# Kernel tuning notes

Measured on AMD Instinct MI355X. Metric: run time of the kernel, lower is better.

Reference implementation:

```python
import jax, jax.numpy as jnp
import numpy as np

N_NODES = 50000
N_EDGES = 600000
D_IN = 128
D_HID = 128
N_IDX = 4096


def gcn_conv(x, W, b, edge_index, num_nodes):
    """PyG GCNConv: add self loops, symmetric deg normalization, scatter-add, bias."""
    h = x @ W  # [N, D_out]
    loop = jnp.arange(num_nodes, dtype=edge_index.dtype)
    src = jnp.concatenate([edge_index[0], loop])
    dst = jnp.concatenate([edge_index[1], loop])
    deg = jax.ops.segment_sum(jnp.ones_like(dst, dtype=h.dtype), dst, num_segments=num_nodes)
    dinv = jnp.where(deg > 0, jax.lax.rsqrt(jnp.maximum(deg, 1.0)), 0.0)
    norm = dinv[src] * dinv[dst]  # [E+N]
    msgs = h[src] * norm[:, None]
    out = jax.ops.segment_sum(msgs, dst, num_segments=num_nodes)
    return out + b


def setup_inputs() -> dict:
    key = jax.random.key(0)
    ks = jax.random.split(key, 18)
    d = {
        "x": jax.random.normal(ks[0], (N_NODES, D_IN), dtype=jnp.float32),
        "syntactic_edge_index": jax.random.randint(ks[1], (2, N_EDGES), 0, N_NODES, dtype=jnp.int32),
        "sequential_edge_index": jax.random.randint(ks[2], (2, N_EDGES), 0, N_NODES, dtype=jnp.int32),
        "semantic_edge_index": jax.random.randint(ks[3], (2, N_EDGES), 0, N_NODES, dtype=jnp.int32),
        "index": jax.random.randint(ks[4], (N_IDX,), 0, N_NODES, dtype=jnp.int32),
    }
    s = 1.0 / np.sqrt(D_IN)
    names = ["syn", "seq", "sem"]
    for i, n in enumerate(names):
        d[f"w1_{n}"] = jax.random.uniform(ks[5 + i], (D_IN, D_HID), jnp.float32, -s, s)
        d[f"b1_{n}"] = jnp.zeros((D_HID,), jnp.float32)
        d[f"w2_{n}"] = jax.random.uniform(ks[8 + i], (D_HID, D_HID), jnp.float32, -s, s)
        d[f"b2_{n}"] = jnp.zeros((D_HID,), jnp.float32)
    return d


def reference(x, syntactic_edge_index, sequential_edge_index, semantic_edge_index, index,
              w1_syn, b1_syn, w1_seq, b1_seq, w1_sem, b1_sem,
              w2_syn, b2_syn, w2_seq, b2_seq, w2_sem, b2_sem):
    n = x.shape[0]
    # layer 1: three parallel GCN branches + ReLU (dropout is identity in eval mode)
    a = jax.nn.relu(gcn_conv(x, w1_syn, b1_syn, syntactic_edge_index, n))
    b = jax.nn.relu(gcn_conv(x, w1_seq, b1_seq, sequential_edge_index, n))
    c = jax.nn.relu(gcn_conv(x, w1_sem, b1_sem, semantic_edge_index, n))
    h = jnp.maximum(jnp.maximum(a, b), c)
    # layer 2
    a2 = jax.nn.relu(gcn_conv(h, w2_syn, b2_syn, syntactic_edge_index, n))
    b2 = jax.nn.relu(gcn_conv(h, w2_seq, b2_seq, sequential_edge_index, n))
    c2 = jax.nn.relu(gcn_conv(h, w2_sem, b2_sem, semantic_edge_index, n))
    out = jnp.maximum(jnp.maximum(a2, b2), c2)
    return out[index]
```

## Files before the change

kernel.cpp:

```cpp
#include <hip/hip_runtime.h>
#include <hip/hip_fp16.h>

#define NN 50000
#define NE 600000
#define NG 3
#define D  128
#define NI 4096
#define BW 1024
#define NBUCK 49
#define EPT_BIN 16
#define EPB_BIN (256 * EPT_BIN)
#define NBLK_BIN ((NE + EPB_BIN - 1) / EPB_BIN)
#define XCVT_BLKS 3125
#define WCVT_BLKS 48
#define CNT_BLKS (NBLK_BIN * NG)

typedef _Float16 half8 __attribute__((ext_vector_type(8)));
typedef _Float16 half4v __attribute__((ext_vector_type(4)));
typedef float floatx4 __attribute__((ext_vector_type(4)));

static __device__ __forceinline__ float wextract(unsigned int v) {
  unsigned short u = (unsigned short)(v >> 16);
  _Float16 h;
  __builtin_memcpy(&h, &u, 2);
  return (float)h;
}

static __device__ __forceinline__ unsigned int packsw(int s, float w) {
  _Float16 h = (_Float16)w;
  unsigned short u;
  __builtin_memcpy(&u, &h, 2);
  return (unsigned int)s | ((unsigned int)u << 16);
}


__global__ __launch_bounds__(256) void prep_kernel(
    const float* __restrict__ x, __half* __restrict__ xh,
    const float* __restrict__ W0, const float* __restrict__ W1, const float* __restrict__ W2,
    const float* __restrict__ W3, const float* __restrict__ W4, const float* __restrict__ W5,
    __half* __restrict__ Wf,
    const int* __restrict__ e0, const int* __restrict__ e1, const int* __restrict__ e2,
    int* __restrict__ bucketCnt) {
  __shared__ int cnt[NBUCK];
  int blk = blockIdx.x;
  int tid = threadIdx.x;
  if (blk < XCVT_BLKS) {
    int i = blk * 256 + tid;
    size_t base = (size_t)i * 8;
    float4 v0 = *(const float4*)&x[base];
    float4 v1 = *(const float4*)&x[base + 4];
    half8 h;
    h[0] = (_Float16)v0.x; h[1] = (_Float16)v0.y; h[2] = (_Float16)v0.z; h[3] = (_Float16)v0.w;
    h[4] = (_Float16)v1.x; h[5] = (_Float16)v1.y; h[6] = (_Float16)v1.z; h[7] = (_Float16)v1.w;
    *(half8*)&xh[base] = h;
  } else if (blk < XCVT_BLKS + WCVT_BLKS) {
    const float* Wm[6] = {W0, W1, W2, W3, W4, W5};
    int t = (blk - XCVT_BLKS) * 256 + tid;
    int mat = t >> 11;
    int fr = (t >> 6) & 31;
    int lane = t & 63;
    int tt = fr >> 2, ks = fr & 3;
    int n = tt * 16 + (lane & 15);
    int kb = ks * 32 + (lane >> 4) * 8;
    const float* W = Wm[mat];
#pragma unroll
    for (int j = 0; j < 8; j++)
      Wf[(size_t)t * 8 + j] = __float2half(W[(kb + j) * 128 + n]);
  } else {
    int cb = blk - XCVT_BLKS - WCVT_BLKS;
    int g = cb / NBLK_BIN, eb = cb % NBLK_BIN;
    const int* ei = (g == 0) ? e0 : ((g == 1) ? e1 : e2);
    if (tid < NBUCK) cnt[tid] = 0;
    __syncthreads();
    int base = eb * EPB_BIN;
#pragma unroll
    for (int i = 0; i < EPT_BIN; i++) {
      int e = base + tid + i * 256;
      if (e < NE) atomicAdd(&cnt[ei[NE + e] >> 10], 1);
    }
    __syncthreads();
    if (tid < NBUCK) atomicAdd(&bucketCnt[g * NBUCK + tid], cnt[tid]);
  }
}

__global__ void bscan_kernel(const int* __restrict__ bucketCnt, int* __restrict__ bucketBase,
                             int* __restrict__ cursor, int* __restrict__ rp) {
  int g = threadIdx.x >> 6;
  int lane = threadIdx.x & 63;
  if (g >= NG) return;
  int v = (lane < NBUCK) ? bucketCnt[g * NBUCK + lane] : 0;
  int incl = v;
#pragma unroll
  for (int off = 1; off < 64; off <<= 1) {
    int t = __shfl_up(incl, off, 64);
    if (lane >= off) incl += t;
  }
  int ex = incl - v;
  if (lane < NBUCK) {
    bucketBase[g * NBUCK + lane] = ex;
    cursor[g * NBUCK + lane] = ex;
  }
  if (lane == 0) rp[g * (NN + 1) + NN] = NE;
}

__global__ __launch_bounds__(256) void bin_kernel(const int* __restrict__ e0,
    const int* __restrict__ e1, const int* __restrict__ e2,
    int* __restrict__ cursor, unsigned int* __restrict__ binned) {
  __shared__ int cnt[4][NBUCK];
  __shared__ int base[NBUCK];
  __shared__ int woff[4][NBUCK];
  int g = blockIdx.y;
  const int* ei = (g == 0) ? e0 : ((g == 1) ? e1 : e2);
  int tid = threadIdx.x;
  int wave = tid >> 6;
  if (tid < NBUCK) { cnt[0][tid] = 0; cnt[1][tid] = 0; cnt[2][tid] = 0; cnt[3][tid] = 0; }
  __syncthreads();
  int estart = blockIdx.x * EPB_BIN;
  int src[EPT_BIN], dst[EPT_BIN], rk[EPT_BIN];
#pragma unroll
  for (int i = 0; i < EPT_BIN; i++) {
    int e = estart + tid + i * 256;
    if (e < NE) {
      src[i] = ei[e];
      dst[i] = ei[NE + e];
      rk[i] = atomicAdd(&cnt[wave][dst[i] >> 10], 1);
    } else {
      rk[i] = -1;
    }
  }
  __syncthreads();
  if (tid < NBUCK) {
    int c0 = cnt[0][tid], c1 = cnt[1][tid], c2 = cnt[2][tid], c3 = cnt[3][tid];
    int total = c0 + c1 + c2 + c3;
    base[tid] = (total > 0) ? atomicAdd(&cursor[g * NBUCK + tid], total) : 0;
    woff[0][tid] = 0; woff[1][tid] = c0; woff[2][tid] = c0 + c1; woff[3][tid] = c0 + c1 + c2;
  }
  __syncthreads();
#pragma unroll
  for (int i = 0; i < EPT_BIN; i++) {
    if (rk[i] >= 0) {
      int b = dst[i] >> 10;
      binned[(size_t)g * NE + base[b] + woff[wave][b] + rk[i]] =
          (unsigned int)src[i] | ((unsigned int)dst[i] << 16);
    }
  }
}

__global__ __launch_bounds__(256) void csr_kernel(const unsigned int* __restrict__ binned,
    const int* __restrict__ bucketBase, const int* __restrict__ bucketCnt,
    int* __restrict__ rp, float* __restrict__ dinv) {
  __shared__ int deg[BW];
  __shared__ int wsum[4];
  int g = blockIdx.y, b = blockIdx.x;
  int tid = threadIdx.x;
  int node0 = b * BW;
  int bb = bucketBase[g * NBUCK + b];
  int total = bucketCnt[g * NBUCK + b];
  const unsigned int* bp = binned + (size_t)g * NE + bb;
  for (int i = tid; i < BW; i += 256) deg[i] = 0;
  __syncthreads();
  for (int e = tid; e < total; e += 256) {
    unsigned int p = bp[e];
    atomicAdd(&deg[(int)(p >> 16) - node0], 1);
  }
  __syncthreads();
  int d0 = deg[tid * 4], d1 = deg[tid * 4 + 1], d2 = deg[tid * 4 + 2], d3 = deg[tid * 4 + 3];
  int s = d0 + d1 + d2 + d3;
  int lane = tid & 63;
  int incl = s;
#pragma unroll
  for (int off = 1; off < 64; off <<= 1) {
    int n = __shfl_up(incl, off, 64);
    if (lane >= off) incl += n;
  }
  if (lane == 63) wsum[tid >> 6] = incl;
  __syncthreads();
  int wbase = 0;
#pragma unroll
  for (int w = 0; w < 4; w++)
    if (w < (tid >> 6)) wbase += wsum[w];
  int ex = wbase + incl - s;
  int exs[4] = {ex, ex + d0, ex + d0 + d1, ex + d0 + d1 + d2};
  int ds[4] = {d0, d1, d2, d3};
#pragma unroll
  for (int k = 0; k < 4; k++) {
    int node = node0 + tid * 4 + k;
    if (node < NN) {
      rp[g * (NN + 1) + node] = bb + exs[k];
      dinv[g * NN + node] = rsqrtf((float)ds[k] + 1.0f);
    }
  }
}

__global__ __launch_bounds__(256) void fillp_kernel(const unsigned int* __restrict__ binned,
    const int* __restrict__ bucketBase, const int* __restrict__ bucketCnt,
    const int* __restrict__ rp, const float* __restrict__ dinv,
    unsigned int* __restrict__ colp) {
  __shared__ int cur[BW];
  int g = blockIdx.y, b = blockIdx.x;
  int tid = threadIdx.x;
  int node0 = b * BW;
  int bb = bucketBase[g * NBUCK + b];
  int total = bucketCnt[g * NBUCK + b];
  const unsigned int* bp = binned + (size_t)g * NE + bb;
  for (int i = tid; i < BW; i += 256) {
    int node = node0 + i;
    cur[i] = (node < NN) ? rp[g * (NN + 1) + node] : 0;
  }
  __syncthreads();
  for (int e = tid; e < total; e += 256) {
    unsigned int p = bp[e];
    int srcid = (int)(p & 0xffffu);
    int r = atomicAdd(&cur[(int)(p >> 16) - node0], 1);
    colp[(size_t)g * NE + r] = packsw(srcid, dinv[g * NN + srcid]);
  }
}


__global__ __launch_bounds__(256) void aggb_kernel(
    const __half* __restrict__ srch, const int* __restrict__ rp,
    const unsigned int* __restrict__ colp, const float* __restrict__ dinv,
    const int* __restrict__ index, __half* __restrict__ tout, int nrows) {
  int b = blockIdx.y;
  int lane = threadIdx.x & 63;
  int grp = lane >> 4;
  int l16 = lane & 15;
  int gb = grp << 4;
  int wv = (blockIdx.x * 256 + threadIdx.x) >> 6;
  int w = wv * 4 + grp;
  int valid = (w < nrows);
  int wc = valid ? w : 0;
  int node = index ? index[wc] : wc;
  const _Float16* srcv = (const _Float16*)srch;
  const int* rpb = rp + b * (NN + 1);
  int s = rpb[node];
  int e = rpb[node + 1];
  int n = valid ? (e - s) : 0;
  float di = dinv[b * NN + node];
  half8 selfh = *(const half8*)&srcv[(size_t)node * D + l16 * 8];
  float a[8];
#pragma unroll
  for (int k = 0; k < 8; k++) a[k] = di * (float)selfh[k];
  int nmax = n;
  nmax = max(nmax, __shfl_xor(nmax, 16, 64));
  nmax = max(nmax, __shfl_xor(nmax, 32, 64));
  const unsigned int* cp = colp + (size_t)b * NE;
  for (int j0 = 0; j0 < nmax; j0 += 16) {
    unsigned int c = (j0 + l16 < n) ? cp[s + j0 + l16] : 0u;
    int rem = nmax - j0;
    rem = (rem > 16) ? 16 : rem;
    for (int jj = 0; jj < rem; jj += 4) {
      unsigned int v0 = (unsigned int)__shfl((int)c, gb + jj + 0, 64);
      unsigned int v1 = (unsigned int)__shfl((int)c, gb + jj + 1, 64);
      unsigned int v2 = (unsigned int)__shfl((int)c, gb + jj + 2, 64);
      unsigned int v3 = (unsigned int)__shfl((int)c, gb + jj + 3, 64);
      half8 h0 = *(const half8*)&srcv[(size_t)(v0 & 0xffffu) * D + l16 * 8];
      half8 h1 = *(const half8*)&srcv[(size_t)(v1 & 0xffffu) * D + l16 * 8];
      half8 h2 = *(const half8*)&srcv[(size_t)(v2 & 0xffffu) * D + l16 * 8];
      half8 h3 = *(const half8*)&srcv[(size_t)(v3 & 0xffffu) * D + l16 * 8];
      float w0 = wextract(v0), w1 = wextract(v1);
      float w2 = wextract(v2), w3 = wextract(v3);
#pragma unroll
      for (int k = 0; k < 8; k++) a[k] = fmaf((float)h0[k], w0, a[k]);
#pragma unroll
      for (int k = 0; k < 8; k++) a[k] = fmaf((float)h1[k], w1, a[k]);
#pragma unroll
      for (int k = 0; k < 8; k++) a[k] = fmaf((float)h2[k], w2, a[k]);
#pragma unroll
      for (int k = 0; k < 8; k++) a[k] = fmaf((float)h3[k], w3, a[k]);
    }
  }
  if (valid) {
    half8 o;
#pragma unroll
    for (int k = 0; k < 8; k++) o[k] = (_Float16)(di * a[k]);
    _Float16* tv = (_Float16*)tout;
    *(half8*)&tv[(size_t)b * nrows * D + (size_t)w * D + l16 * 8] = o;
  }
}


#define ALD 136

__global__ __launch_bounds__(256) void mmf_kernel(const __half* __restrict__ A,
    const __half* __restrict__ Wf,
    const float* __restrict__ B0, const float* __restrict__ B1, const float* __restrict__ B2,
    __half* __restrict__ outh, float* __restrict__ outf, int M) {
  __shared__ _Float16 As[128 * ALD];
  __shared__ _Float16 Ws[16384];
  const float* Bb[3] = {B0, B1, B2};
  const int tid = threadIdx.x;
  const int wave = tid >> 6, lane = tid & 63;
  const int wr = (wave >> 1) * 64, wc = (wave & 1) * 64;
  const int ln = lane & 15, quad = lane >> 4;
  const int row0 = blockIdx.x * 128;
  float om[4][4][4];

  for (int b = 0; b < 3; b++) {
    const __half* Wb = Wf + (size_t)b * 16384;
#pragma unroll
    for (int i = 0; i < 8; i++) {
      int id = tid + i * 256;
      *(half8*)&Ws[id * 8] = *(const half8*)&Wb[(size_t)id * 8];
    }
    const __half* Ab = A + (size_t)b * M * D;
#pragma unroll
    for (int i = 0; i < 8; i++) {
      int idx = tid + i * 256;
      int r = idx >> 4, c8 = idx & 15;
      int gr = row0 + r;
      gr = (gr < M) ? gr : (M - 1);
      half8 v = *(const half8*)&Ab[(size_t)gr * D + c8 * 8];
      *(half8*)&As[r * ALD + c8 * 8] = v;
    }
    __syncthreads();

    float bias[4];
#pragma unroll
    for (int ct = 0; ct < 4; ct++) bias[ct] = Bb[b][wc + ct * 16 + ln];
    floatx4 acc[4][4];
#pragma unroll
    for (int rt = 0; rt < 4; rt++)
#pragma unroll
      for (int ct = 0; ct < 4; ct++)
        acc[rt][ct] = (floatx4){bias[ct], bias[ct], bias[ct], bias[ct]};

#pragma unroll
    for (int ks = 0; ks < 4; ks++) {
      half8 av[4];
#pragma unroll
      for (int rt = 0; rt < 4; rt++)
        av[rt] = *(const half8*)&As[(wr + rt * 16 + ln) * ALD + ks * 32 + quad * 8];
#pragma unroll
      for (int ct = 0; ct < 4; ct++) {
        int tt = (wc >> 4) + ct;
        half8 bv = *(const half8*)&Ws[((tt * 4 + ks) * 64 + lane) * 8];
#pragma unroll
        for (int rt = 0; rt < 4; rt++)
          acc[rt][ct] = __builtin_amdgcn_mfma_f32_16x16x32_f16(av[rt], bv, acc[rt][ct], 0, 0, 0);
      }
    }
#pragma unroll
    for (int rt = 0; rt < 4; rt++)
#pragma unroll
      for (int ct = 0; ct < 4; ct++)
#pragma unroll
        for (int r = 0; r < 4; r++) {
          float v = fmaxf(acc[rt][ct][r], 0.f);
          om[rt][ct][r] = (b == 0) ? v : fmaxf(om[rt][ct][r], v);
        }
    __syncthreads();
  }
#pragma unroll
  for (int rt = 0; rt < 4; rt++) {
    int m = row0 + wr + rt * 16 + quad * 4;
#pragma unroll
    for (int r = 0; r < 4; r++) {
      if (m + r < M) {
#pragma unroll
        for (int ct = 0; ct < 4; ct++) {
          int n = wc + ct * 16 + ln;
          if (outh) outh[(size_t)(m + r) * D + n] = __float2half(om[rt][ct][r]);
          else      outf[(size_t)(m + r) * D + n] = om[rt][ct][r];
        }
      }
    }
  }
}


extern "C" void kernel_launch(void* const* d_in, const int* in_sizes, int n_in,
                              void* d_out, int out_size, void* d_ws, size_t ws_size,
                              hipStream_t stream) {
  const float* x = (const float*)d_in[0];
  const int* e0 = (const int*)d_in[1];
  const int* e1 = (const int*)d_in[2];
  const int* e2 = (const int*)d_in[3];
  const int* index = (const int*)d_in[4];
  const float* w1[3] = {(const float*)d_in[5], (const float*)d_in[9],  (const float*)d_in[13]};
  const float* b1[3] = {(const float*)d_in[6], (const float*)d_in[10], (const float*)d_in[14]};
  const float* w2[3] = {(const float*)d_in[7], (const float*)d_in[11], (const float*)d_in[15]};
  const float* b2[3] = {(const float*)d_in[8], (const float*)d_in[12], (const float*)d_in[16]};
  float* out = (float*)d_out;

  char* ws = (char*)d_ws;
  size_t o = 0;
  auto alloc = [&](size_t bytes) {
    o = (o + 255) & ~(size_t)255;
    void* p = ws + o;
    o += bytes;
    return p;
  };
  int*    rp     = (int*)alloc((size_t)NG * (NN + 1) * 4);
  unsigned int* colp = (unsigned int*)alloc((size_t)NG * NE * 4);
  float*  dinv   = (float*)alloc((size_t)NG * NN * 4);
  int*    bcnt   = (int*)alloc((size_t)NG * NBUCK * 4);
  int*    bbase  = (int*)alloc((size_t)NG * NBUCK * 4);
  int*    bcur   = (int*)alloc((size_t)NG * NBUCK * 4);
  __half* xh     = (__half*)alloc((size_t)NN * D * 2);
  __half* Wf     = (__half*)alloc((size_t)6 * 128 * 128 * 2);
  __half* t1     = (__half*)alloc((size_t)NG * NN * D * 2);
  __half* hacc   = (__half*)alloc((size_t)NN * D * 2);
  unsigned int* binned = (unsigned int*)t1;
  __half* t2     = t1;
  (void)ws_size; (void)in_sizes; (void)n_in; (void)out_size;

  hipMemsetAsync(bcnt, 0, (size_t)NG * NBUCK * 4, stream);
  prep_kernel<<<XCVT_BLKS + WCVT_BLKS + CNT_BLKS, 256, 0, stream>>>(
      x, xh, w1[0], w1[1], w1[2], w2[0], w2[1], w2[2], Wf, e0, e1, e2, bcnt);
  bscan_kernel<<<1, 192, 0, stream>>>(bcnt, bbase, bcur, rp);
  bin_kernel<<<dim3(NBLK_BIN, NG), 256, 0, stream>>>(e0, e1, e2, bcur, binned);
  csr_kernel<<<dim3(NBUCK, NG), 256, 0, stream>>>(binned, bbase, bcnt, rp, dinv);
  fillp_kernel<<<dim3(NBUCK, NG), 256, 0, stream>>>(binned, bbase, bcnt, rp, dinv, colp);

  aggb_kernel<<<dim3((NN + 15) / 16, NG), 256, 0, stream>>>(
      xh, rp, colp, dinv, nullptr, t1, NN);
  mmf_kernel<<<(NN + 127) / 128, 256, 0, stream>>>(t1, Wf, b1[0], b1[1], b1[2],
                                                   hacc, nullptr, NN);
  aggb_kernel<<<dim3((NI + 15) / 16, NG), 256, 0, stream>>>(
      hacc, rp, colp, dinv, index, t2, NI);
  mmf_kernel<<<(NI + 127) / 128, 256, 0, stream>>>(t2, Wf + (size_t)3 * 16384,
                                                   b2[0], b2[1], b2[2], nullptr, out, NI);
}
```

Before: 275.6 us.

## Replace bucket binning CSR build with global-atomic degree count and direct scatter

Removes the intermediate bucket-binning pass and its binned buffer. Per-node in-degree is now counted with global atomics inside the prep kernel, and the CSR scan reads that count directly. A new scatter kernel places each edge into its CSR slot using global atomics on per-node cursors and a precomputed fp16 dinv. This cuts one kernel and one full edge pass, but it trades bucket-local shared-memory atomics for scattered global atomics and uncoalesced writes, and edge order within each row becomes nondeterministic.

```diff
diff --git a/kernel.cpp b/kernel.cpp
--- a/kernel.cpp
+++ b/kernel.cpp
@@ -8,15 +8,17 @@
 #define NI 4096
 #define BW 1024
 #define NBUCK 49
+#define NPAD (NBUCK * BW)
 #define EPT_BIN 16
 #define EPB_BIN (256 * EPT_BIN)
 #define NBLK_BIN ((NE + EPB_BIN - 1) / EPB_BIN)
 #define XCVT_BLKS 3125
 #define WCVT_BLKS 48
 #define CNT_BLKS (NBLK_BIN * NG)
+#define EPT_SC 8
+#define NBLK_SC ((NE + 256 * EPT_SC - 1) / (256 * EPT_SC))
 
 typedef _Float16 half8 __attribute__((ext_vector_type(8)));
-typedef _Float16 half4v __attribute__((ext_vector_type(4)));
 typedef float floatx4 __attribute__((ext_vector_type(4)));
 
 static __device__ __forceinline__ float wextract(unsigned int v) {
@@ -24,13 +26,6 @@
   _Float16 h;
   __builtin_memcpy(&h, &u, 2);
   return (float)h;
-}
-
-static __device__ __forceinline__ unsigned int packsw(int s, float w) {
-  _Float16 h = (_Float16)w;
-  unsigned short u;
-  __builtin_memcpy(&u, &h, 2);
-  return (unsigned int)s | ((unsigned int)u << 16);
 }
 
 
@@ -40,7 +35,7 @@
     const float* __restrict__ W3, const float* __restrict__ W4, const float* __restrict__ W5,
     __half* __restrict__ Wf,
     const int* __restrict__ e0, const int* __restrict__ e1, const int* __restrict__ e2,
-    int* __restrict__ bucketCnt) {
+    int* __restrict__ bucketCnt, int* __restrict__ deg) {
   __shared__ int cnt[NBUCK];
   int blk = blockIdx.x;
   int tid = threadIdx.x;
@@ -76,7 +71,11 @@
 #pragma unroll
     for (int i = 0; i < EPT_BIN; i++) {
       int e = base + tid + i * 256;
-      if (e < NE) atomicAdd(&cnt[ei[NE + e] >> 10], 1);
+      if (e < NE) {
+        int dst = ei[NE + e];
+        atomicAdd(&cnt[dst >> 10], 1);
+        atomicAdd(&deg[g * NPAD + dst], 1);
+      }
     }
     __syncthreads();
     if (tid < NBUCK) atomicAdd(&bucketCnt[g * NBUCK + tid], cnt[tid]);
@@ -84,7 +83,7 @@
 }
 
 __global__ void bscan_kernel(const int* __restrict__ bucketCnt, int* __restrict__ bucketBase,
-                             int* __restrict__ cursor, int* __restrict__ rp) {
+                             int* __restrict__ rp) {
   int g = threadIdx.x >> 6;
   int lane = threadIdx.x & 63;
   if (g >= NG) return;
@@ -96,75 +95,20 @@
     if (lane >= off) incl += t;
   }
   int ex = incl - v;
-  if (lane < NBUCK) {
-    bucketBase[g * NBUCK + lane] = ex;
-    cursor[g * NBUCK + lane] = ex;
-  }
+  if (lane < NBUCK) bucketBase[g * NBUCK + lane] = ex;
   if (lane == 0) rp[g * (NN + 1) + NN] = NE;
 }
 
-__global__ __launch_bounds__(256) void bin_kernel(const int* __restrict__ e0,
-    const int* __restrict__ e1, const int* __restrict__ e2,
-    int* __restrict__ cursor, unsigned int* __restrict__ binned) {
-  __shared__ int cnt[4][NBUCK];
-  __shared__ int base[NBUCK];
-  __shared__ int woff[4][NBUCK];
-  int g = blockIdx.y;
-  const int* ei = (g == 0) ? e0 : ((g == 1) ? e1 : e2);
-  int tid = threadIdx.x;
-  int wave = tid >> 6;
-  if (tid < NBUCK) { cnt[0][tid] = 0; cnt[1][tid] = 0; cnt[2][tid] = 0; cnt[3][tid] = 0; }
-  __syncthreads();
-  int estart = blockIdx.x * EPB_BIN;
-  int src[EPT_BIN], dst[EPT_BIN], rk[EPT_BIN];
-#pragma unroll
-  for (int i = 0; i < EPT_BIN; i++) {
-    int e = estart + tid + i * 256;
-    if (e < NE) {
-      src[i] = ei[e];
-      dst[i] = ei[NE + e];
-      rk[i] = atomicAdd(&cnt[wave][dst[i] >> 10], 1);
-    } else {
-      rk[i] = -1;
-    }
-  }
-  __syncthreads();
-  if (tid < NBUCK) {
-    int c0 = cnt[0][tid], c1 = cnt[1][tid], c2 = cnt[2][tid], c3 = cnt[3][tid];
-    int total = c0 + c1 + c2 + c3;
-    base[tid] = (total > 0) ? atomicAdd(&cursor[g * NBUCK + tid], total) : 0;
-    woff[0][tid] = 0; woff[1][tid] = c0; woff[2][tid] = c0 + c1; woff[3][tid] = c0 + c1 + c2;
-  }
-  __syncthreads();
-#pragma unroll
-  for (int i = 0; i < EPT_BIN; i++) {
-    if (rk[i] >= 0) {
-      int b = dst[i] >> 10;
-      binned[(size_t)g * NE + base[b] + woff[wave][b] + rk[i]] =
-          (unsigned int)src[i] | ((unsigned int)dst[i] << 16);
-    }
-  }
-}
-
-__global__ __launch_bounds__(256) void csr_kernel(const unsigned int* __restrict__ binned,
-    const int* __restrict__ bucketBase, const int* __restrict__ bucketCnt,
-    int* __restrict__ rp, float* __restrict__ dinv) {
-  __shared__ int deg[BW];
+__global__ __launch_bounds__(256) void csr_kernel(const int* __restrict__ deg,
+    const int* __restrict__ bucketBase, int* __restrict__ rp, float* __restrict__ dinv,
+    unsigned short* __restrict__ dinvh, int* __restrict__ cur) {
   __shared__ int wsum[4];
   int g = blockIdx.y, b = blockIdx.x;
   int tid = threadIdx.x;
   int node0 = b * BW;
   int bb = bucketBase[g * NBUCK + b];
-  int total = bucketCnt[g * NBUCK + b];
-  const unsigned int* bp = binned + (size_t)g * NE + bb;
-  for (int i = tid; i < BW; i += 256) deg[i] = 0;
-  __syncthreads();
-  for (int e = tid; e < total; e += 256) {
-    unsigned int p = bp[e];
-    atomicAdd(&deg[(int)(p >> 16) - node0], 1);
-  }
-  __syncthreads();
-  int d0 = deg[tid * 4], d1 = deg[tid * 4 + 1], d2 = deg[tid * 4 + 2], d3 = deg[tid * 4 + 3];
+  int4 dv = *(const int4*)&deg[(size_t)g * NPAD + node0 + tid * 4];
+  int d0 = dv.x, d1 = dv.y, d2 = dv.z, d3 = dv.w;
   int s = d0 + d1 + d2 + d3;
   int lane = tid & 63;
   int incl = s;
@@ -186,34 +130,43 @@
   for (int k = 0; k < 4; k++) {
     int node = node0 + tid * 4 + k;
     if (node < NN) {
-      rp[g * (NN + 1) + node] = bb + exs[k];
-      dinv[g * NN + node] = rsqrtf((float)ds[k] + 1.0f);
-    }
-  }
-}
-
-__global__ __launch_bounds__(256) void fillp_kernel(const unsigned int* __restrict__ binned,
-    const int* __restrict__ bucketBase, const int* __restrict__ bucketCnt,
-    const int* __restrict__ rp, const float* __restrict__ dinv,
+      int r = bb + exs[k];
+      rp[g * (NN + 1) + node] = r;
+      cur[g * NN + node] = r;
+      float di = rsqrtf((float)ds[k] + 1.0f);
+      dinv[g * NN + node] = di;
+      _Float16 h = (_Float16)di;
+      unsigned short u;
+      __builtin_memcpy(&u, &h, 2);
+      dinvh[g * NN + node] = u;
+    }
+  }
+}
+
+__global__ __launch_bounds__(256) void scatter_kernel(const int* __restrict__ e0,
+    const int* __restrict__ e1, const int* __restrict__ e2,
+    const unsigned short* __restrict__ dinvh, int* __restrict__ cur,
     unsigned int* __restrict__ colp) {
-  __shared__ int cur[BW];
-  int g = blockIdx.y, b = blockIdx.x;
-  int tid = threadIdx.x;
-  int node0 = b * BW;
-  int bb = bucketBase[g * NBUCK + b];
-  int total = bucketCnt[g * NBUCK + b];
-  const unsigned int* bp = binned + (size_t)g * NE + bb;
-  for (int i = tid; i < BW; i += 256) {
-    int node = node0 + i;
-    cur[i] = (node < NN) ? rp[g * (NN + 1) + node] : 0;
-  }
-  __syncthreads();
-  for (int e = tid; e < total; e += 256) {
-    unsigned int p = bp[e];
-    int srcid = (int)(p & 0xffffu);
-    int r = atomicAdd(&cur[(int)(p >> 16) - node0], 1);
-    colp[(size_t)g * NE + r] = packsw(srcid, dinv[g * NN + srcid]);
-  }
+  int g = blockIdx.y;
+  const int* ei = (g == 0) ? e0 : ((g == 1) ? e1 : e2);
+  int e = (blockIdx.x * 256 + threadIdx.x) * EPT_SC;
+  if (e >= NE) return;
+  int4 sa = *(const int4*)&ei[e];
+  int4 sb = *(const int4*)&ei[e + 4];
+  int4 da = *(const int4*)&ei[NE + e];
+  int4 db = *(const int4*)&ei[NE + e + 4];
+  int src[8] = {sa.x, sa.y, sa.z, sa.w, sb.x, sb.y, sb.z, sb.w};
+  int dst[8] = {da.x, da.y, da.z, da.w, db.x, db.y, db.z, db.w};
+  int rk[8];
+#pragma unroll
+  for (int j = 0; j < 8; j++) rk[j] = atomicAdd(&cur[g * NN + dst[j]], 1);
+  unsigned int pw[8];
+#pragma unroll
+  for (int j = 0; j < 8; j++)
+    pw[j] = (unsigned int)src[j] | ((unsigned int)dinvh[g * NN + src[j]] << 16);
+  unsigned int* cg = colp + (size_t)g * NE;
+#pragma unroll
+  for (int j = 0; j < 8; j++) cg[rk[j]] = pw[j];
 }
 
 
@@ -394,24 +347,24 @@
   int*    rp     = (int*)alloc((size_t)NG * (NN + 1) * 4);
   unsigned int* colp = (unsigned int*)alloc((size_t)NG * NE * 4);
   float*  dinv   = (float*)alloc((size_t)NG * NN * 4);
-  int*    bcnt   = (int*)alloc((size_t)NG * NBUCK * 4);
+  unsigned short* dinvh = (unsigned short*)alloc((size_t)NG * NN * 2);
+  int*    deg    = (int*)alloc((size_t)NG * NPAD * 4 + (size_t)NG * NBUCK * 4);
+  int*    bcnt   = deg + (size_t)NG * NPAD;
   int*    bbase  = (int*)alloc((size_t)NG * NBUCK * 4);
-  int*    bcur   = (int*)alloc((size_t)NG * NBUCK * 4);
+  int*    cur    = (int*)alloc((size_t)NG * NN * 4);
   __half* xh     = (__half*)alloc((size_t)NN * D * 2);
   __half* Wf     = (__half*)alloc((size_t)6 * 128 * 128 * 2);
   __half* t1     = (__half*)alloc((size_t)NG * NN * D * 2);
   __half* hacc   = (__half*)alloc((size_t)NN * D * 2);
-  unsigned int* binned = (unsigned int*)t1;
   __half* t2     = t1;
   (void)ws_size; (void)in_sizes; (void)n_in; (void)out_size;
 
-  hipMemsetAsync(bcnt, 0, (size_t)NG * NBUCK * 4, stream);
+  hipMemsetAsync(deg, 0, (size_t)NG * NPAD * 4 + (size_t)NG * NBUCK * 4, stream);
   prep_kernel<<<XCVT_BLKS + WCVT_BLKS + CNT_BLKS, 256, 0, stream>>>(
-      x, xh, w1[0], w1[1], w1[2], w2[0], w2[1], w2[2], Wf, e0, e1, e2, bcnt);
-  bscan_kernel<<<1, 192, 0, stream>>>(bcnt, bbase, bcur, rp);
-  bin_kernel<<<dim3(NBLK_BIN, NG), 256, 0, stream>>>(e0, e1, e2, bcur, binned);
-  csr_kernel<<<dim3(NBUCK, NG), 256, 0, stream>>>(binned, bbase, bcnt, rp, dinv);
-  fillp_kernel<<<dim3(NBUCK, NG), 256, 0, stream>>>(binned, bbase, bcnt, rp, dinv, colp);
+      x, xh, w1[0], w1[1], w1[2], w2[0], w2[1], w2[2], Wf, e0, e1, e2, bcnt, deg);
+  bscan_kernel<<<1, 192, 0, stream>>>(bcnt, bbase, rp);
+  csr_kernel<<<dim3(NBUCK, NG), 256, 0, stream>>>(deg, bbase, rp, dinv, dinvh, cur);
+  scatter_kernel<<<dim3(NBLK_SC, NG), 256, 0, stream>>>(e0, e1, e2, dinvh, cur, colp);
 
   aggb_kernel<<<dim3((NN + 15) / 16, NG), 256, 0, stream>>>(
       xh, rp, colp, dinv, nullptr, t1, NN);
```

Result: slower. 444.7 us (+61.3%).

## Compute per-node degrees globally up front and merge CSR and fill kernels

Applied to the files above, without the earlier changes.

The prep kernel now counts per-node degrees with global atomics instead of per-bucket shared histograms. A new kernel derives dinv, a half-precision dinv copy and the bucket counts from those degrees. The CSR row-pointer and fill passes become one kernel that reads the precomputed degrees rather than re-counting them from the binned edges, which removes a kernel launch and one pass over the binned edges. The cost is global atomic traffic on 1.8M edges spread across 150K counters, an extra small kernel, and padded buffers.

```diff
diff --git a/kernel.cpp b/kernel.cpp
--- a/kernel.cpp
+++ b/kernel.cpp
@@ -8,15 +8,16 @@
 #define NI 4096
 #define BW 1024
 #define NBUCK 49
+#define NPAD (NBUCK * BW)
 #define EPT_BIN 16
 #define EPB_BIN (256 * EPT_BIN)
 #define NBLK_BIN ((NE + EPB_BIN - 1) / EPB_BIN)
 #define XCVT_BLKS 3125
 #define WCVT_BLKS 48
 #define CNT_BLKS (NBLK_BIN * NG)
+#define DINV_BLKS (NG * NBUCK)
 
 typedef _Float16 half8 __attribute__((ext_vector_type(8)));
-typedef _Float16 half4v __attribute__((ext_vector_type(4)));
 typedef float floatx4 __attribute__((ext_vector_type(4)));
 
 static __device__ __forceinline__ float wextract(unsigned int v) {
@@ -26,11 +27,11 @@
   return (float)h;
 }
 
-static __device__ __forceinline__ unsigned int packsw(int s, float w) {
-  _Float16 h = (_Float16)w;
+static __device__ __forceinline__ unsigned short h16(float f) {
+  _Float16 h = (_Float16)f;
   unsigned short u;
   __builtin_memcpy(&u, &h, 2);
-  return (unsigned int)s | ((unsigned int)u << 16);
+  return u;
 }
 
 
@@ -40,8 +41,7 @@
     const float* __restrict__ W3, const float* __restrict__ W4, const float* __restrict__ W5,
     __half* __restrict__ Wf,
     const int* __restrict__ e0, const int* __restrict__ e1, const int* __restrict__ e2,
-    int* __restrict__ bucketCnt) {
-  __shared__ int cnt[NBUCK];
+    int* __restrict__ deg) {
   int blk = blockIdx.x;
   int tid = threadIdx.x;
   if (blk < XCVT_BLKS) {
@@ -70,17 +70,38 @@
     int cb = blk - XCVT_BLKS - WCVT_BLKS;
     int g = cb / NBLK_BIN, eb = cb % NBLK_BIN;
     const int* ei = (g == 0) ? e0 : ((g == 1) ? e1 : e2);
-    if (tid < NBUCK) cnt[tid] = 0;
-    __syncthreads();
+    int* dg = deg + (size_t)g * NPAD;
     int base = eb * EPB_BIN;
 #pragma unroll
     for (int i = 0; i < EPT_BIN; i++) {
       int e = base + tid + i * 256;
-      if (e < NE) atomicAdd(&cnt[ei[NE + e] >> 10], 1);
-    }
-    __syncthreads();
-    if (tid < NBUCK) atomicAdd(&bucketCnt[g * NBUCK + tid], cnt[tid]);
-  }
+      if (e < NE) atomicAdd(&dg[ei[NE + e]], 1);
+    }
+  }
+}
+
+__global__ __launch_bounds__(256) void dinvcnt_kernel(const int* __restrict__ deg,
+    float* __restrict__ dinv, unsigned short* __restrict__ dinvh,
+    int* __restrict__ bucketCnt) {
+  __shared__ int wred[4];
+  size_t base = (size_t)blockIdx.x * BW + threadIdx.x * 4;
+  int4 dv = *(const int4*)&deg[base];
+  float4 f;
+  f.x = rsqrtf((float)dv.x + 1.0f);
+  f.y = rsqrtf((float)dv.y + 1.0f);
+  f.z = rsqrtf((float)dv.z + 1.0f);
+  f.w = rsqrtf((float)dv.w + 1.0f);
+  *(float4*)&dinv[base] = f;
+  ushort4 u;
+  u.x = h16(f.x); u.y = h16(f.y); u.z = h16(f.z); u.w = h16(f.w);
+  *(ushort4*)&dinvh[base] = u;
+  int s = dv.x + dv.y + dv.z + dv.w;
+#pragma unroll
+  for (int off = 32; off >= 1; off >>= 1) s += __shfl_down(s, off, 64);
+  if ((threadIdx.x & 63) == 0) wred[threadIdx.x >> 6] = s;
+  __syncthreads();
+  if (threadIdx.x == 0)
+    bucketCnt[blockIdx.x] = wred[0] + wred[1] + wred[2] + wred[3];
 }
 
 __global__ void bscan_kernel(const int* __restrict__ bucketCnt, int* __restrict__ bucketBase,
@@ -146,25 +167,18 @@
   }
 }
 
-__global__ __launch_bounds__(256) void csr_kernel(const unsigned int* __restrict__ binned,
-    const int* __restrict__ bucketBase, const int* __restrict__ bucketCnt,
-    int* __restrict__ rp, float* __restrict__ dinv) {
-  __shared__ int deg[BW];
+__global__ __launch_bounds__(256) void csrf_kernel(const unsigned int* __restrict__ binned,
+    const int* __restrict__ bucketBase, const int* __restrict__ deg,
+    const unsigned short* __restrict__ dinvh,
+    int* __restrict__ rp, unsigned int* __restrict__ colp) {
+  __shared__ int cur[BW];
   __shared__ int wsum[4];
   int g = blockIdx.y, b = blockIdx.x;
   int tid = threadIdx.x;
   int node0 = b * BW;
   int bb = bucketBase[g * NBUCK + b];
-  int total = bucketCnt[g * NBUCK + b];
-  const unsigned int* bp = binned + (size_t)g * NE + bb;
-  for (int i = tid; i < BW; i += 256) deg[i] = 0;
-  __syncthreads();
-  for (int e = tid; e < total; e += 256) {
-    unsigned int p = bp[e];
-    atomicAdd(&deg[(int)(p >> 16) - node0], 1);
-  }
-  __syncthreads();
-  int d0 = deg[tid * 4], d1 = deg[tid * 4 + 1], d2 = deg[tid * 4 + 2], d3 = deg[tid * 4 + 3];
+  int4 dv = *(const int4*)&deg[(size_t)g * NPAD + node0 + tid * 4];
+  int d0 = dv.x, d1 = dv.y, d2 = dv.z, d3 = dv.w;
   int s = d0 + d1 + d2 + d3;
   int lane = tid & 63;
   int incl = s;
@@ -181,38 +195,22 @@
     if (w < (tid >> 6)) wbase += wsum[w];
   int ex = wbase + incl - s;
   int exs[4] = {ex, ex + d0, ex + d0 + d1, ex + d0 + d1 + d2};
-  int ds[4] = {d0, d1, d2, d3};
 #pragma unroll
   for (int k = 0; k < 4; k++) {
     int node = node0 + tid * 4 + k;
-    if (node < NN) {
-      rp[g * (NN + 1) + node] = bb + exs[k];
-      dinv[g * NN + node] = rsqrtf((float)ds[k] + 1.0f);
-    }
-  }
-}
-
-__global__ __launch_bounds__(256) void fillp_kernel(const unsigned int* __restrict__ binned,
-    const int* __restrict__ bucketBase, const int* __restrict__ bucketCnt,
-    const int* __restrict__ rp, const float* __restrict__ dinv,
-    unsigned int* __restrict__ colp) {
-  __shared__ int cur[BW];
-  int g = blockIdx.y, b = blockIdx.x;
-  int tid = threadIdx.x;
-  int node0 = b * BW;
-  int bb = bucketBase[g * NBUCK + b];
-  int total = bucketCnt[g * NBUCK + b];
+    cur[tid * 4 + k] = bb + exs[k];
+    if (node < NN) rp[g * (NN + 1) + node] = bb + exs[k];
+  }
+  int total = wsum[0] + wsum[1] + wsum[2] + wsum[3];
+  __syncthreads();
   const unsigned int* bp = binned + (size_t)g * NE + bb;
-  for (int i = tid; i < BW; i += 256) {
-    int node = node0 + i;
-    cur[i] = (node < NN) ? rp[g * (NN + 1) + node] : 0;
-  }
-  __syncthreads();
+  const unsigned short* dh = dinvh + (size_t)g * NPAD;
+  unsigned int* cg = colp + (size_t)g * NE;
   for (int e = tid; e < total; e += 256) {
     unsigned int p = bp[e];
     int srcid = (int)(p & 0xffffu);
     int r = atomicAdd(&cur[(int)(p >> 16) - node0], 1);
-    colp[(size_t)g * NE + r] = packsw(srcid, dinv[g * NN + srcid]);
+    cg[r] = (unsigned int)srcid | ((unsigned int)dh[srcid] << 16);
   }
 }
 
@@ -236,7 +234,7 @@
   int s = rpb[node];
   int e = rpb[node + 1];
   int n = valid ? (e - s) : 0;
-  float di = dinv[b * NN + node];
+  float di = dinv[b * NPAD + node];
   half8 selfh = *(const half8*)&srcv[(size_t)node * D + l16 * 8];
   float a[8];
 #pragma unroll
@@ -393,7 +391,9 @@
   };
   int*    rp     = (int*)alloc((size_t)NG * (NN + 1) * 4);
   unsigned int* colp = (unsigned int*)alloc((size_t)NG * NE * 4);
-  float*  dinv   = (float*)alloc((size_t)NG * NN * 4);
+  int*    deg    = (int*)alloc((size_t)NG * NPAD * 4);
+  float*  dinv   = (float*)alloc((size_t)NG * NPAD * 4);
+  unsigned short* dinvh = (unsigned short*)alloc((size_t)NG * NPAD * 2);
   int*    bcnt   = (int*)alloc((size_t)NG * NBUCK * 4);
   int*    bbase  = (int*)alloc((size_t)NG * NBUCK * 4);
   int*    bcur   = (int*)alloc((size_t)NG * NBUCK * 4);
@@ -405,13 +405,13 @@
   __half* t2     = t1;
   (void)ws_size; (void)in_sizes; (void)n_in; (void)out_size;
 
-  hipMemsetAsync(bcnt, 0, (size_t)NG * NBUCK * 4, stream);
+  hipMemsetAsync(deg, 0, (size_t)NG * NPAD * 4, stream);
   prep_kernel<<<XCVT_BLKS + WCVT_BLKS + CNT_BLKS, 256, 0, stream>>>(
-      x, xh, w1[0], w1[1], w1[2], w2[0], w2[1], w2[2], Wf, e0, e1, e2, bcnt);
+      x, xh, w1[0], w1[1], w1[2], w2[0], w2[1], w2[2], Wf, e0, e1, e2, deg);
+  dinvcnt_kernel<<<DINV_BLKS, 256, 0, stream>>>(deg, dinv, dinvh, bcnt);
   bscan_kernel<<<1, 192, 0, stream>>>(bcnt, bbase, bcur, rp);
   bin_kernel<<<dim3(NBLK_BIN, NG), 256, 0, stream>>>(e0, e1, e2, bcur, binned);
-  csr_kernel<<<dim3(NBUCK, NG), 256, 0, stream>>>(binned, bbase, bcnt, rp, dinv);
-  fillp_kernel<<<dim3(NBUCK, NG), 256, 0, stream>>>(binned, bbase, bcnt, rp, dinv, colp);
+  csrf_kernel<<<dim3(NBUCK, NG), 256, 0, stream>>>(binned, bbase, deg, dinvh, rp, colp);
 
   aggb_kernel<<<dim3((NN + 15) / 16, NG), 256, 0, stream>>>(
       xh, rp, colp, dinv, nullptr, t1, NN);
```

Measured after the change: 344.1 us. +24.8%, slower.
